# Performance work log

Measured on AMD Instinct MI355X. Metric: run time of the kernel, lower is better.

Reference implementation:

```python
import jax, jax.numpy as jnp
import numpy as np

N_NODES = 50000
N_EDGES = 800000
IN_C = 128
OUT_C = 128
HEADS = 1
BN_EPS = 1e-5


def setup_inputs() -> dict:
    key = jax.random.key(0)
    k1, k2, k3, k4, k5 = jax.random.split(key, 5)
    x = jax.random.normal(k1, (N_NODES, IN_C), dtype=jnp.float32)
    embedding = jax.random.normal(k2, (N_NODES, OUT_C), dtype=jnp.float32)
    # edges with no self loops (module strips then re-adds self loops)
    dst = jax.random.randint(k3, (N_EDGES,), 0, N_NODES)
    off = jax.random.randint(k4, (N_EDGES,), 1, N_NODES)
    src = (dst + off) % N_NODES
    edge_index = jnp.stack([src, dst]).astype(jnp.int64)
    # parameters
    W = jax.random.normal(k5, (HEADS * OUT_C, IN_C), dtype=jnp.float32) * (1.0 / np.sqrt(IN_C))
    bias = jnp.zeros((HEADS * OUT_C,), dtype=jnp.float32)
    gamma = jnp.ones((HEADS * OUT_C,), dtype=jnp.float32)
    beta = jnp.zeros((HEADS * OUT_C,), dtype=jnp.float32)
    return {"x": x, "edge_index": edge_index, "embedding": embedding,
            "W": W, "bias": bias, "gamma": gamma, "beta": beta}


def reference(x, edge_index, embedding, W, bias, gamma, beta):
    N = x.shape[0]
    xl = x @ W.T  # [N, H*C]
    # add self loops (input edges contain none)
    loop = jnp.arange(N, dtype=edge_index.dtype)
    src = jnp.concatenate([edge_index[0], loop])  # j (source)
    dst = jnp.concatenate([edge_index[1], loop])  # i (target / aggregation index)
    # per-edge attention: cosine-sim style embedding dot product (scalar, shared over heads)
    alpha = jnp.sum(embedding[dst] * embedding[src], axis=-1)  # [Etot]
    # segment softmax over destination neighborhoods
    amax = jax.ops.segment_max(alpha, dst, num_segments=N)
    e = jnp.exp(alpha - amax[dst])
    denom = jax.ops.segment_sum(e, dst, num_segments=N)
    a = e / (denom[dst] + 1e-16)  # [Etot]
    # gather-scale-scatter aggregation
    msg = xl[src] * a[:, None]  # [Etot, H*C]
    out = jax.ops.segment_sum(msg, dst, num_segments=N) + bias  # [N, H*C]
    # BatchNorm1d (training mode: batch stats, biased variance) + ReLU
    mu = out.mean(axis=0)
    var = jnp.mean((out - mu) ** 2, axis=0)
    out = (out - mu) * jax.lax.rsqrt(var + BN_EPS) * gamma + beta
    return jnp.maximum(out, 0.0)
```

## Files before the change

### kernel.cpp

```cpp
#include <hip/hip_runtime.h>
#include <math.h>

#define C 128

typedef _Float16 f16x8 __attribute__((ext_vector_type(8)));
typedef _Float16 half2_t __attribute__((ext_vector_type(2)));
typedef __attribute__((ext_vector_type(4))) float f32x4;

static __device__ __forceinline__ unsigned int pkh2(float lo, float hi) {
    unsigned short l = __builtin_bit_cast(unsigned short, (_Float16)lo);
    unsigned short h = __builtin_bit_cast(unsigned short, (_Float16)hi);
    return ((unsigned int)h << 16) | l;
}
static __device__ __forceinline__ float h2f_lo(unsigned int u) {
    return (float)__builtin_bit_cast(_Float16, (unsigned short)(u & 0xFFFFu));
}
static __device__ __forceinline__ float h2f_hi(unsigned int u) {
    return (float)__builtin_bit_cast(_Float16, (unsigned short)(u >> 16));
}
static __device__ __forceinline__ float dot2acc(unsigned int a, unsigned int b, float c) {
#if __has_builtin(__builtin_amdgcn_fdot2)
    return __builtin_amdgcn_fdot2(__builtin_bit_cast(half2_t, a),
                                  __builtin_bit_cast(half2_t, b), c, false);
#else
    c = fmaf(h2f_lo(a), h2f_lo(b), c);
    return fmaf(h2f_hi(a), h2f_hi(b), c);
#endif
}

__global__ __launch_bounds__(256) void k_stageA(const float* __restrict__ x,
                                                const float* __restrict__ Wf0,
                                                unsigned short* __restrict__ xlh,
                                                const float* __restrict__ embf,
                                                unsigned int* __restrict__ embh,
                                                const int* __restrict__ eidx,
                                                int* __restrict__ binCounts,
                                                int N, int E,
                                                int nGemmBlocks, int nCastBlocks,
                                                int totalA8) {
    __shared__ int lh[256];
    const int b = blockIdx.x;

    if (b < nGemmBlocks) {
        __shared__ unsigned int wsh[C * C / 2];
        const int tid = threadIdx.x;
        for (int i = tid; i < C * C / 8; i += 256) {
            const float4 a = ((const float4*)Wf0)[i * 2];
            const float4 bb = ((const float4*)Wf0)[i * 2 + 1];
            uint4 o;
            o.x = pkh2(a.x, a.y); o.y = pkh2(a.z, a.w);
            o.z = pkh2(bb.x, bb.y); o.w = pkh2(bb.z, bb.w);
            ((uint4*)wsh)[i] = o;
        }
        __syncthreads();

        const int lane = threadIdx.x & 63;
        const int wave = threadIdx.x >> 6;
        const int row0 = b * 64 + wave * 16;
        const int r = lane & 15, kg = lane >> 4;

        int arow = row0 + r;
        if (arow >= N) arow = N - 1;
        const float* xrow = x + (size_t)arow * C;
        f16x8 A[4];
#pragma unroll
        for (int kb = 0; kb < 4; ++kb) {
            const float4 p0 = ((const float4*)(xrow + kb * 32 + kg * 8))[0];
            const float4 p1 = ((const float4*)(xrow + kb * 32 + kg * 8))[1];
            f16x8 a;
            a[0] = (_Float16)p0.x; a[1] = (_Float16)p0.y;
            a[2] = (_Float16)p0.z; a[3] = (_Float16)p0.w;
            a[4] = (_Float16)p1.x; a[5] = (_Float16)p1.y;
            a[6] = (_Float16)p1.z; a[7] = (_Float16)p1.w;
            A[kb] = a;
        }

#pragma unroll
        for (int nt = 0; nt < 8; ++nt) {
            const uint4* wrow = (const uint4*)wsh + (size_t)(nt * 16 + r) * 16;
            f32x4 acc = {0.0f, 0.0f, 0.0f, 0.0f};
#pragma unroll
            for (int kb = 0; kb < 4; ++kb) {
                f16x8 B = __builtin_bit_cast(f16x8, wrow[kb * 4 + kg]);
                acc = __builtin_amdgcn_mfma_f32_16x16x32_f16(A[kb], B, acc, 0, 0, 0);
            }
            const int orow = row0 + kg * 4;
            const int ocol = nt * 16 + r;
#pragma unroll
            for (int i = 0; i < 4; ++i)
                if (orow + i < N)
                    xlh[(size_t)(orow + i) * C + ocol] =
                        __builtin_bit_cast(unsigned short, (_Float16)acc[i]);
        }
    } else if (b < nGemmBlocks + nCastBlocks) {
        int i = (b - nGemmBlocks) * 256 + threadIdx.x;
        if (i >= totalA8) return;
        const float4 a = ((const float4*)embf)[i * 2];
        const float4 bb = ((const float4*)embf)[i * 2 + 1];
        uint4 o;
        o.x = pkh2(a.x, a.y); o.y = pkh2(a.z, a.w);
        o.z = pkh2(bb.x, bb.y); o.w = pkh2(bb.z, bb.w);
        ((uint4*)embh)[i] = o;
    } else {
        const int t = threadIdx.x;
        lh[t] = 0;
        __syncthreads();
        const int base = (b - nGemmBlocks - nCastBlocks) * 2048;
#pragma unroll
        for (int j = 0; j < 8; ++j) {
            const int e = base + j * 256 + t;
            if (e < E) atomicAdd(&lh[eidx[E + e] >> 8], 1);
        }
        __syncthreads();
        const int v = lh[t];
        if (v) atomicAdd(&binCounts[t], v);
    }
}

__global__ __launch_bounds__(256) void k_bin(const int* __restrict__ eidx,
                                             const int* __restrict__ binCounts,
                                             int* __restrict__ binAlloc,
                                             unsigned int* __restrict__ binned, int E) {
    __shared__ int lh[256];
    __shared__ int sc[256];
    __shared__ int lb[256];
    const int t = threadIdx.x;
    const int v = binCounts[t];
    lh[t] = 0;
    sc[t] = v;
    __syncthreads();
    const int base = blockIdx.x * 2048;
    int bj[8], rj[8];
    unsigned int recj[8];
#pragma unroll
    for (int j = 0; j < 8; ++j) {
        const int e = base + j * 256 + t;
        bj[j] = -1;
        if (e < E) {
            const int s = eidx[e];
            const int d = eidx[E + e];
            bj[j] = d >> 8;
            recj[j] = ((unsigned)(d & 255) << 24) | (unsigned)s;
            rj[j] = atomicAdd(&lh[bj[j]], 1);
        }
    }
    __syncthreads();
    for (int o = 1; o < 256; o <<= 1) {
        int u = (t >= o) ? sc[t - o] : 0;
        __syncthreads();
        sc[t] += u;
        __syncthreads();
    }
    const int excl = sc[t] - v;
    const int c = lh[t];
    if (c) lb[t] = excl + atomicAdd(&binAlloc[t], c);
    __syncthreads();
#pragma unroll
    for (int j = 0; j < 8; ++j) {
        if (bj[j] >= 0) binned[lb[bj[j]] + rj[j]] = recj[j];
    }
}

__global__ __launch_bounds__(256) void k_place(const unsigned int* __restrict__ binned,
                                               const int* __restrict__ binCounts,
                                               int* __restrict__ offs,
                                               int* __restrict__ src_s,
                                               int N, int E, int NB) {
    __shared__ int sc[256];
    __shared__ int cnt[256];
    __shared__ int ts[256];
    __shared__ int cur[256];
    __shared__ int r0s, r1s;
    const int b = blockIdx.x;
    const int t = threadIdx.x;
    const int node0 = b * 256;
    const int v0 = binCounts[t];
    sc[t] = v0;
    cnt[t] = 0;
    __syncthreads();
    for (int o = 1; o < 256; o <<= 1) {
        int u = (t >= o) ? sc[t - o] : 0;
        __syncthreads();
        sc[t] += u;
        __syncthreads();
    }
    if (t == b) { r0s = sc[t] - v0; r1s = sc[t]; }
    __syncthreads();
    const int r0 = r0s, r1 = r1s;
    for (int i = r0 + t; i < r1; i += 256)
        atomicAdd(&cnt[binned[i] >> 24], 1);
    __syncthreads();
    const int v = cnt[t];
    ts[t] = v;
    __syncthreads();
    for (int o = 1; o < 256; o <<= 1) {
        int u = (t >= o) ? ts[t - o] : 0;
        __syncthreads();
        ts[t] += u;
        __syncthreads();
    }
    const int excl = r0 + ts[t] - v;
    if (node0 + t < N) offs[node0 + t] = excl;
    cur[t] = excl;
    __syncthreads();
    for (int i = r0 + t; i < r1; i += 256) {
        const unsigned int rec = binned[i];
        const int pos = atomicAdd(&cur[rec >> 24], 1);
        src_s[pos] = (int)(rec & 0xFFFFFFu);
    }
    if (b == NB - 1 && t == 0) offs[N] = E;
}

__global__ __launch_bounds__(256) void k_agg(const unsigned int* __restrict__ xlh,
                                             const unsigned int* __restrict__ embh,
                                             const int* __restrict__ src_s,
                                             const int* __restrict__ offs,
                                             const float* __restrict__ bias,
                                             float* __restrict__ out,
                                             float* __restrict__ psum,
                                             float* __restrict__ psq, int N) {
    const int node = (int)((blockIdx.x * (size_t)blockDim.x + threadIdx.x) >> 6);
    const int lane = threadIdx.x & 63;
    const int wave = threadIdx.x >> 6;
    const bool active = node < N;
    float2 o2 = {0.0f, 0.0f};

    if (active) {
        const int g = lane >> 3;
        const int sl = lane & 7;
        const int s0 = offs[node], s1 = offs[node + 1];

        const uint4* erow = (const uint4*)(embh + (size_t)node * (C / 2));
        const uint4 e0 = erow[sl * 2], e1 = erow[sl * 2 + 1];

        float p = 0.0f;
        p = dot2acc(e0.x, e0.x, p); p = dot2acc(e0.y, e0.y, p);
        p = dot2acc(e0.z, e0.z, p); p = dot2acc(e0.w, e0.w, p);
        p = dot2acc(e1.x, e1.x, p); p = dot2acc(e1.y, e1.y, p);
        p = dot2acc(e1.z, e1.z, p); p = dot2acc(e1.w, e1.w, p);
        p += __shfl_xor(p, 4); p += __shfl_xor(p, 2); p += __shfl_xor(p, 1);

        float m = p;
        float wself = 1.0f;
        float dex = 0.0f;
        float dpart = 0.0f;
        const unsigned int xw = xlh[(size_t)node * (C / 2) + lane];
        float2 acc = {h2f_lo(xw), h2f_hi(xw)};

        for (int base = s0; base < s1; base += 64) {
            int mys = -1;
            if (base + lane < s1) mys = src_s[base + lane];
            const int iters = min(8, (s1 - base + 7) >> 3);
            for (int k = 0; k < iters; ++k) {
                const int sg = __shfl(mys, k * 8 + g);
                const int sa = (sg >= 0) ? sg : node;

                const uint4* vrow = (const uint4*)(embh + (size_t)sa * (C / 2));
                const uint4 v0 = vrow[sl * 2], v1 = vrow[sl * 2 + 1];
                float a = 0.0f;
                a = dot2acc(e0.x, v0.x, a); a = dot2acc(e0.y, v0.y, a);
                a = dot2acc(e0.z, v0.z, a); a = dot2acc(e0.w, v0.w, a);
                a = dot2acc(e1.x, v1.x, a); a = dot2acc(e1.y, v1.y, a);
                a = dot2acc(e1.z, v1.z, a); a = dot2acc(e1.w, v1.w, a);
                a += __shfl_xor(a, 4); a += __shfl_xor(a, 2); a += __shfl_xor(a, 1);

                const bool valid = sg >= 0;
                const bool hot = valid && (a > m - 28.0f);
                if (__any(hot)) {
                    const unsigned long long bal = __ballot(hot);
#pragma unroll 1
                    for (int j = 0; j < 8; ++j) {
                        if (!((bal >> (j * 8)) & 1ULL)) continue;
                        const float aj = __shfl(a, j * 8);
                        const int sj = __shfl(mys, k * 8 + j);
                        if (aj > m) {
                            const float cs = __expf(m - aj);
                            dpart *= cs; dex *= cs; wself *= cs;
                            acc.x *= cs; acc.y *= cs;
                            m = aj;
                        }
                        const float w = __expf(aj - m);
                        dex += w;
                        if (w > 1e-12f) {
                            const unsigned int u = xlh[(size_t)sj * (C / 2) + lane];
                            acc.x = fmaf(w, h2f_lo(u), acc.x);
                            acc.y = fmaf(w, h2f_hi(u), acc.y);
                        }
                    }
                }
                dpart += (valid && !hot) ? __expf(a - m) : 0.0f;
            }
        }

        float dg = dpart;
        dg += __shfl_xor(dg, 8); dg += __shfl_xor(dg, 16); dg += __shfl_xor(dg, 32);
        const float dtot = wself + dex + dg;
        const float inv = 1.0f / (dtot + 1e-16f);
        const int c = lane * 2;
        o2.x = fmaf(acc.x, inv, bias[c]);
        o2.y = fmaf(acc.y, inv, bias[c + 1]);
        ((float2*)(out + (size_t)node * C))[lane] = o2;
    }

    __shared__ float2 lsum[256];
    __shared__ float2 lsq[256];
    lsum[threadIdx.x] = o2;
    float2 q2v;
    q2v.x = o2.x * o2.x;
    q2v.y = o2.y * o2.y;
    lsq[threadIdx.x] = q2v;
    __syncthreads();
    if (wave == 0) {
        float2 S = lsum[lane], Q = lsq[lane];
#pragma unroll
        for (int j = 1; j < 4; ++j) {
            const float2 a = lsum[j * 64 + lane];
            const float2 b = lsq[j * 64 + lane];
            S.x += a.x; S.y += a.y;
            Q.x += b.x; Q.y += b.y;
        }
        const int slot = ((int)blockIdx.x & 63) * C + lane * 2;
        atomicAdd(&psum[slot],     S.x);
        atomicAdd(&psum[slot + 1], S.y);
        atomicAdd(&psq[slot],      Q.x);
        atomicAdd(&psq[slot + 1],  Q.y);
    }
}

__global__ __launch_bounds__(128) void k_bnreduce(const float* __restrict__ psum,
                                                  const float* __restrict__ psq,
                                                  float* __restrict__ ssum,
                                                  float* __restrict__ ssq) {
    const int t = threadIdx.x;
    float S = 0.0f, Q = 0.0f;
#pragma unroll 4
    for (int b = 0; b < 64; ++b) {
        S += psum[b * C + t];
        Q += psq[b * C + t];
    }
    ssum[t] = S;
    ssq[t] = Q;
}

__global__ __launch_bounds__(256) void k_bnapply(float* __restrict__ out,
                                                 const float* __restrict__ ssum,
                                                 const float* __restrict__ ssq,
                                                 const float* __restrict__ gamma,
                                                 const float* __restrict__ beta,
                                                 int N) {
    const int idx = blockIdx.x * blockDim.x + threadIdx.x;
    const int total = N * (C / 4);
    if (idx >= total) return;
    const int c = (idx * 4) & 127;
    float4 v = ((const float4*)out)[idx];
    const float invN = 1.0f / (float)N;
    float r[4] = {v.x, v.y, v.z, v.w};
#pragma unroll
    for (int j = 0; j < 4; ++j) {
        float mu = ssum[c + j] * invN;
        float var = fmaf(-mu, mu, ssq[c + j] * invN);
        var = fmaxf(var, 0.0f);
        float sc = gamma[c + j] / sqrtf(var + 1e-5f);
        float val = fmaf(r[j] - mu, sc, beta[c + j]);
        r[j] = fmaxf(val, 0.0f);
    }
    float4 o = {r[0], r[1], r[2], r[3]};
    ((float4*)out)[idx] = o;
}

extern "C" void kernel_launch(void* const* d_in, const int* in_sizes, int n_in,
                              void* d_out, int out_size, void* d_ws, size_t ws_size,
                              hipStream_t stream) {
    const float* x     = (const float*)d_in[0];
    const int*   eidx  = (const int*)d_in[1];
    const float* emb   = (const float*)d_in[2];
    const float* W     = (const float*)d_in[3];
    const float* bias  = (const float*)d_in[4];
    const float* gamma = (const float*)d_in[5];
    const float* beta  = (const float*)d_in[6];
    const int N = in_sizes[0] / C;
    const int E = in_sizes[1] / 2;
    float* out = (float*)d_out;

    char* ws = (char*)d_ws;
    size_t off = 0;
    auto alloc = [&](size_t bytes) -> void* {
        void* p = ws + off;
        off = (off + bytes + 255) & ~(size_t)255;
        return p;
    };
    unsigned short* xlh  = (unsigned short*)alloc((size_t)N * C * 2);
    unsigned int*   embh = (unsigned int*)  alloc((size_t)N * C * 2);
    int*   src_s    = (int*)  alloc((size_t)E * 4);
    unsigned int* binned = (unsigned int*)alloc((size_t)E * 4);
    int*   offs     = (int*)  alloc((size_t)(N + 1) * 4);
    float* ssum     = (float*)alloc(C * 4);
    float* ssq      = (float*)alloc(C * 4);
    char*  zbase    = (char*)alloc(0);
    int*   binCounts= (int*)  alloc(256 * 4);
    int*   binAlloc = (int*)  alloc(256 * 4);
    float* psum     = (float*)alloc(64 * C * 4);
    float* psq      = (float*)alloc(64 * C * 4);
    size_t zbytes   = (char*)ws + off - zbase;

    const int NB = (N + 255) / 256;
    const int nEdgeBlocks = (E + 2047) / 2048;
    const int embTot8 = N * (C / 8);
    const int nGemmBlocks = (N + 63) / 64;
    const int nCastBlocks = (embTot8 + 255) / 256;

    hipMemsetAsync(zbase, 0, zbytes, stream);

    k_stageA <<<nGemmBlocks + nCastBlocks + nEdgeBlocks, 256, 0, stream>>>(
                 x, W, xlh, emb, embh, eidx, binCounts,
                 N, E, nGemmBlocks, nCastBlocks, embTot8);
    k_bin    <<<nEdgeBlocks,     256, 0, stream>>>(eidx, binCounts, binAlloc, binned, E);
    k_place  <<<NB,              256, 0, stream>>>(binned, binCounts, offs, src_s, N, E, NB);
    k_agg    <<<(int)(((size_t)N * 64 + 255) / 256), 256, 0, stream>>>(
                 (const unsigned int*)xlh, embh, src_s, offs, bias, out,
                 psum, psq, N);
    k_bnreduce<<<1,              128, 0, stream>>>(psum, psq, ssum, ssq);
    k_bnapply<<<(N * (C / 4) + 255) / 256, 256, 0, stream>>>(out, ssum, ssq, gamma, beta, N);
}
```

Baseline: 121.2 us.

## Prefetch next embedding row in agg loop and fuse BN reduce into apply

In the aggregation kernel, the embedding row for the next neighbor group is loaded before computing the current dot product, a software-pipelined prefetch that hides gather latency. Separately, the single-block BN reduction kernel is removed; each block of a 512-block grid-stride bnapply kernel now redundantly reduces the 64 partial sums into shared-memory scale/shift values before normalizing. This saves a launch and the per-element recomputation of rsqrt, at the cost of redundant partial reads per block and extra registers in the agg loop.

```diff
diff --git a/kernel.cpp b/kernel.cpp
--- a/kernel.cpp
+++ b/kernel.cpp
@@ -251,20 +251,34 @@
             int mys = -1;
             if (base + lane < s1) mys = src_s[base + lane];
             const int iters = min(8, (s1 - base + 7) >> 3);
+
+            int sgc = __shfl(mys, g);
+            {
+                const int sac = (sgc >= 0) ? sgc : node;
+            }
+            const uint4* vrc = (const uint4*)(embh +
+                                (size_t)((sgc >= 0) ? sgc : node) * (C / 2));
+            uint4 v0c = vrc[sl * 2], v1c = vrc[sl * 2 + 1];
+
             for (int k = 0; k < iters; ++k) {
-                const int sg = __shfl(mys, k * 8 + g);
-                const int sa = (sg >= 0) ? sg : node;
-
-                const uint4* vrow = (const uint4*)(embh + (size_t)sa * (C / 2));
-                const uint4 v0 = vrow[sl * 2], v1 = vrow[sl * 2 + 1];
+                int sgn = -1;
+                uint4 v0n, v1n;
+                if (k + 1 < iters) {
+                    sgn = __shfl(mys, (k + 1) * 8 + g);
+                    const uint4* vrn = (const uint4*)(embh +
+                                        (size_t)((sgn >= 0) ? sgn : node) * (C / 2));
+                    v0n = vrn[sl * 2];
+                    v1n = vrn[sl * 2 + 1];
+                }
+
                 float a = 0.0f;
-                a = dot2acc(e0.x, v0.x, a); a = dot2acc(e0.y, v0.y, a);
-                a = dot2acc(e0.z, v0.z, a); a = dot2acc(e0.w, v0.w, a);
-                a = dot2acc(e1.x, v1.x, a); a = dot2acc(e1.y, v1.y, a);
-                a = dot2acc(e1.z, v1.z, a); a = dot2acc(e1.w, v1.w, a);
+                a = dot2acc(e0.x, v0c.x, a); a = dot2acc(e0.y, v0c.y, a);
+                a = dot2acc(e0.z, v0c.z, a); a = dot2acc(e0.w, v0c.w, a);
+                a = dot2acc(e1.x, v1c.x, a); a = dot2acc(e1.y, v1c.y, a);
+                a = dot2acc(e1.z, v1c.z, a); a = dot2acc(e1.w, v1c.w, a);
                 a += __shfl_xor(a, 4); a += __shfl_xor(a, 2); a += __shfl_xor(a, 1);
 
-                const bool valid = sg >= 0;
+                const bool valid = sgc >= 0;
                 const bool hot = valid && (a > m - 28.0f);
                 if (__any(hot)) {
                     const unsigned long long bal = __ballot(hot);
@@ -289,6 +303,10 @@
                     }
                 }
                 dpart += (valid && !hot) ? __expf(a - m) : 0.0f;
+
+                sgc = sgn;
+                v0c = v0n;
+                v1c = v1n;
             }
         }
 
@@ -327,45 +345,43 @@
     }
 }
 
-__global__ __launch_bounds__(128) void k_bnreduce(const float* __restrict__ psum,
-                                                  const float* __restrict__ psq,
-                                                  float* __restrict__ ssum,
-                                                  float* __restrict__ ssq) {
-    const int t = threadIdx.x;
-    float S = 0.0f, Q = 0.0f;
-#pragma unroll 4
-    for (int b = 0; b < 64; ++b) {
-        S += psum[b * C + t];
-        Q += psq[b * C + t];
-    }
-    ssum[t] = S;
-    ssq[t] = Q;
-}
-
 __global__ __launch_bounds__(256) void k_bnapply(float* __restrict__ out,
-                                                 const float* __restrict__ ssum,
-                                                 const float* __restrict__ ssq,
+                                                 const float* __restrict__ psum,
+                                                 const float* __restrict__ psq,
                                                  const float* __restrict__ gamma,
                                                  const float* __restrict__ beta,
                                                  int N) {
-    const int idx = blockIdx.x * blockDim.x + threadIdx.x;
-    const int total = N * (C / 4);
-    if (idx >= total) return;
-    const int c = (idx * 4) & 127;
-    float4 v = ((const float4*)out)[idx];
-    const float invN = 1.0f / (float)N;
-    float r[4] = {v.x, v.y, v.z, v.w};
-#pragma unroll
-    for (int j = 0; j < 4; ++j) {
-        float mu = ssum[c + j] * invN;
-        float var = fmaf(-mu, mu, ssq[c + j] * invN);
-        var = fmaxf(var, 0.0f);
-        float sc = gamma[c + j] / sqrtf(var + 1e-5f);
-        float val = fmaf(r[j] - mu, sc, beta[c + j]);
-        r[j] = fmaxf(val, 0.0f);
-    }
-    float4 o = {r[0], r[1], r[2], r[3]};
-    ((float4*)out)[idx] = o;
+    __shared__ float smu[C];
+    __shared__ float ssc[C];
+    __shared__ float sbe[C];
+    const int t = threadIdx.x;
+    if (t < C) {
+        float S = 0.0f, Q = 0.0f;
+#pragma unroll 4
+        for (int b = 0; b < 64; ++b) {
+            S += psum[b * C + t];
+            Q += psq[b * C + t];
+        }
+        const float invN = 1.0f / (float)N;
+        const float mu = S * invN;
+        const float var = fmaxf(fmaf(-mu, mu, Q * invN), 0.0f);
+        smu[t] = mu;
+        ssc[t] = gamma[t] / sqrtf(var + 1e-5f);
+        sbe[t] = beta[t];
+    }
+    __syncthreads();
+    const int total4 = N * (C / 4);
+    const int stride = (int)gridDim.x * 256;
+    for (int idx = (int)blockIdx.x * 256 + t; idx < total4; idx += stride) {
+        const int c = (idx * 4) & 127;
+        float4 v = ((const float4*)out)[idx];
+        float r[4] = {v.x, v.y, v.z, v.w};
+#pragma unroll
+        for (int j = 0; j < 4; ++j)
+            r[j] = fmaxf(fmaf(r[j] - smu[c + j], ssc[c + j], sbe[c + j]), 0.0f);
+        float4 o = {r[0], r[1], r[2], r[3]};
+        ((float4*)out)[idx] = o;
+    }
 }
 
 extern "C" void kernel_launch(void* const* d_in, const int* in_sizes, int n_in,
@@ -394,8 +410,6 @@
     int*   src_s    = (int*)  alloc((size_t)E * 4);
     unsigned int* binned = (unsigned int*)alloc((size_t)E * 4);
     int*   offs     = (int*)  alloc((size_t)(N + 1) * 4);
-    float* ssum     = (float*)alloc(C * 4);
-    float* ssq      = (float*)alloc(C * 4);
     char*  zbase    = (char*)alloc(0);
     int*   binCounts= (int*)  alloc(256 * 4);
     int*   binAlloc = (int*)  alloc(256 * 4);
@@ -419,6 +433,5 @@
     k_agg    <<<(int)(((size_t)N * 64 + 255) / 256), 256, 0, stream>>>(
                  (const unsigned int*)xlh, embh, src_s, offs, bias, out,
                  psum, psq, N);
-    k_bnreduce<<<1,              128, 0, stream>>>(psum, psq, ssum, ssq);
-    k_bnapply<<<(N * (C / 4) + 255) / 256, 256, 0, stream>>>(out, ssum, ssq, gamma, beta, N);
-}
+    k_bnapply<<<512,             256, 0, stream>>>(out, psum, psq, gamma, beta, N);
+}
```

Measured after the change: 117.7 us. 1.03x faster.
